# Optimization experiments

Measured on AMD Instinct MI355X. Metric: run time of the kernel, lower is better.

## Reference

```python
import jax, jax.numpy as jnp
import numpy as np

EPS = 1e-5

def layer_norm(x, g, b):
    mu = jnp.mean(x, axis=-1, keepdims=True)
    var = jnp.mean((x - mu) ** 2, axis=-1, keepdims=True)
    return (x - mu) * jax.lax.rsqrt(var + EPS) * g + b

def lstm_scan(x, Wih, Whh, bih, bhh, H):
    # x: [B, T, D]; PyTorch gate order i, f, g, o
    B = x.shape[0]
    gx = jnp.einsum('btd,gd->btg', x, Wih) + bih  # [B, T, 4H]
    gx = jnp.transpose(gx, (1, 0, 2))             # [T, B, 4H]
    def step(carry, g_t):
        h, c = carry
        g = g_t + h @ Whh.T + bhh
        i, f, gg, o = jnp.split(g, 4, axis=-1)
        c = jax.nn.sigmoid(f) * c + jax.nn.sigmoid(i) * jnp.tanh(gg)
        h = jax.nn.sigmoid(o) * jnp.tanh(c)
        return (h, c), h
    h0 = jnp.zeros((B, H), x.dtype)
    (_, _), hs = jax.lax.scan(step, (h0, h0), gx)
    return jnp.transpose(hs, (1, 0, 2))  # [B, T, H]

def gru_last(x, Wih, Whh, bih, bhh, H):
    # x: [B, T, D]; PyTorch gate order r, z, n; returns final hidden [B, H]
    B = x.shape[0]
    gx = jnp.einsum('btd,gd->btg', x, Wih) + bih  # [B, T, 3H]
    gx = jnp.transpose(gx, (1, 0, 2))             # [T, B, 3H]
    def step(h, g_t):
        gh = h @ Whh.T + bhh
        gxr, gxz, gxn = jnp.split(g_t, 3, axis=-1)
        ghr, ghz, ghn = jnp.split(gh, 3, axis=-1)
        r = jax.nn.sigmoid(gxr + ghr)
        z = jax.nn.sigmoid(gxz + ghz)
        n = jnp.tanh(gxn + r * ghn)
        h = (1.0 - z) * n + z * h
        return h, None
    h0 = jnp.zeros((B, H), x.dtype)
    h_last, _ = jax.lax.scan(step, h0, gx)
    return h_last

def setup_inputs() -> dict:
    key = jax.random.key(0)
    ks = jax.random.split(key, 16)
    B, T, D = 512, 512, 128
    H, G, F, C = 128, 128, 160, 64
    s = lambda n: 1.0 / np.sqrt(n)
    u = lambda k, shape, n: jax.random.uniform(k, shape, jnp.float32, -s(n), s(n))
    return {
        'x': jax.random.normal(ks[0], (B, T, D), jnp.float32),
        'lstm_Wih': u(ks[1], (4 * H, D), H), 'lstm_Whh': u(ks[2], (4 * H, H), H),
        'lstm_bih': u(ks[3], (4 * H,), H), 'lstm_bhh': u(ks[4], (4 * H,), H),
        'gru_Wih': u(ks[5], (3 * G, H), G), 'gru_Whh': u(ks[6], (3 * G, G), G),
        'gru_bih': u(ks[7], (3 * G,), G), 'gru_bhh': u(ks[8], (3 * G,), G),
        'ln_lstm_g': jnp.ones((H,), jnp.float32), 'ln_lstm_b': jnp.zeros((H,), jnp.float32),
        'ln_gru_g': jnp.ones((G,), jnp.float32), 'ln_gru_b': jnp.zeros((G,), jnp.float32),
        'fc1_W': u(ks[9], (F, G), G), 'fc1_b': u(ks[10], (F,), G),
        'ln_fc1_g': jnp.ones((F,), jnp.float32), 'ln_fc1_b': jnp.zeros((F,), jnp.float32),
        'fco_W': u(ks[11], (C, F), F), 'fco_b': u(ks[12], (C,), F),
    }

def reference(x, lstm_Wih, lstm_Whh, lstm_bih, lstm_bhh,
              gru_Wih, gru_Whh, gru_bih, gru_bhh,
              ln_lstm_g, ln_lstm_b, ln_gru_g, ln_gru_b,
              fc1_W, fc1_b, ln_fc1_g, ln_fc1_b, fco_W, fco_b):
    H = lstm_Whh.shape[1]
    G = gru_Whh.shape[1]
    lstm_out = lstm_scan(x, lstm_Wih, lstm_Whh, lstm_bih, lstm_bhh, H)  # [B,T,H]
    lstm_out = layer_norm(lstm_out, ln_lstm_g, ln_lstm_b)  # dropout = identity (eval)
    h_last = gru_last(lstm_out, gru_Wih, gru_Whh, gru_bih, gru_bhh, G)  # [B,G]
    h_last = layer_norm(h_last, ln_gru_g, ln_gru_b)
    h_last = jax.nn.relu(h_last)
    z = h_last @ fc1_W.T + fc1_b
    z = jax.nn.relu(layer_norm(z, ln_fc1_g, ln_fc1_b))
    return z @ fco_W.T + fco_b
```

## Files before the change

kernel.cpp:

```cpp
#include <hip/hip_runtime.h>


typedef __attribute__((ext_vector_type(8))) short bf16x8;
typedef __attribute__((ext_vector_type(4))) float f32x4;
typedef __attribute__((ext_vector_type(4))) int i32x4;
typedef unsigned short u16;
typedef unsigned int u32;

#define TT 512
#define HSTR 136

__device__ __forceinline__ u16 f2bf(float f) {
  u32 u = __builtin_bit_cast(u32, f);
  u += 0x7fffu + ((u >> 16) & 1u);
  return (u16)(u >> 16);
}
__device__ __forceinline__ float bf2f(u16 h) {
  return __builtin_bit_cast(float, (u32)h << 16);
}
__device__ __forceinline__ u32 packbf2(float a, float b) {
  return (u32)f2bf(a) | ((u32)f2bf(b) << 16);
}
__device__ __forceinline__ bf16x8 ldg8(const u16* p) {
  return __builtin_bit_cast(bf16x8, *(const i32x4*)p);
}
__device__ __forceinline__ float frcp(float x) { return __builtin_amdgcn_rcpf(x); }
__device__ __forceinline__ float sigm(float x) { return frcp(1.f + __expf(-x)); }
__device__ __forceinline__ float tanh_f(float x) {
  return 1.f - 2.f * frcp(__expf(2.f * x) + 1.f);
}
__device__ __forceinline__ void scan_barrier() {
  __asm__ volatile("" ::: "memory");
  __builtin_amdgcn_s_waitcnt(0xC07F);
  __builtin_amdgcn_s_barrier();
  __asm__ volatile("" ::: "memory");
}
__device__ __forceinline__ void acc_stats(bf16x8 v, float& s1, float& s2) {
#pragma unroll
  for (int j = 0; j < 8; j++) {
    float f = bf2f((u16)v[j]);
    s1 += f;
    s2 = __builtin_fmaf(f, f, s2);
  }
}

__global__ void prep_x(const float* __restrict__ x, u16* __restrict__ xb) {
  size_t i = ((size_t)blockIdx.x * 256 + threadIdx.x) * 4;
  float4 v = *(const float4*)(x + i);
  *(uint2*)(xb + i) = make_uint2(packbf2(v.x, v.y), packbf2(v.z, v.w));
}

__global__ void prep_misc(
    const float* __restrict__ wihl, const float* __restrict__ whhl,
    const float* __restrict__ wihg, const float* __restrict__ whhg,
    const float* __restrict__ bihl, const float* __restrict__ bhhl,
    const float* __restrict__ fc1W, const float* __restrict__ fcoW,
    const float* __restrict__ lnLg, const float* __restrict__ lnLb,
    u16* __restrict__ wihlb, u16* __restrict__ whhlb,
    u16* __restrict__ wihgb, u16* __restrict__ whhgb,
    float* __restrict__ biasl, float* __restrict__ fc1Wt, float* __restrict__ fcoWt,
    float* __restrict__ s1v, float* __restrict__ s2v, u32* __restrict__ flags) {
  int i = blockIdx.x * 256 + threadIdx.x;
  if (i < 65536) {
    wihlb[i] = f2bf(wihl[i]);
  } else if (i < 131072) {
    int k = i - 65536; whhlb[k] = f2bf(whhl[k]);
  } else if (i < 180224) {
    int k = i - 131072;
    wihgb[k] = f2bf(wihg[k] * lnLg[k & 127]);
  } else if (i < 229376) {
    int k = i - 180224; whhgb[k] = f2bf(whhg[k]);
  } else if (i < 229888) {
    int k = i - 229376; biasl[k] = bihl[k] + bhhl[k];
  } else if (i < 250368) {
    int k = i - 229888;
    fc1Wt[k] = fc1W[(k % 160) * 128 + (k / 160)];
  } else if (i < 260608) {
    int k = i - 250368;
    fcoWt[k] = fcoW[(k % 64) * 160 + (k / 64)];
  } else if (i < 260992) {
    int r = i - 260608;
    const float* wr = wihg + r * 128;
    float a = 0.f, b = 0.f;
    for (int j = 0; j < 128; j++) { a += wr[j] * lnLg[j]; b += wr[j] * lnLb[j]; }
    s1v[r] = a; s2v[r] = b;
  } else if (i < 261120) {
    flags[i - 260992] = 0;
  }
}

__global__ __launch_bounds__(512, 2) void scan_pair(
    const u16* __restrict__ xbf,
    const u16* __restrict__ whhl,
    const u16* __restrict__ wihl,
    const float* __restrict__ biasl,
    u16* __restrict__ lout,
    const u16* __restrict__ whhg,
    const u16* __restrict__ wihg,
    const float* __restrict__ gbih, const float* __restrict__ gbhh,
    const float* __restrict__ s1v, const float* __restrict__ s2v,
    float* __restrict__ hlast,
    u32* __restrict__ flags) {
  const int tid = threadIdx.x;
  const int w = tid >> 6, l = tid & 63;
  const int hc = l & 15, q = l >> 4;
  const int col = w * 16 + hc;
  const int pid = blockIdx.x;
  const int grp = ((pid >> 4) << 3) | (pid & 7);
  const int role = (pid >> 3) & 1;
  const int b0 = grp * 4;
  const int mrow = q * 4;
  const int hbase = hc * HSTR + q * 8;

  __shared__ __align__(16) u16 hb0[16 * HSTR];
  __shared__ __align__(16) u16 hb1[16 * HSTR];
  __shared__ float2 stats[2][16];

  for (int i = tid; i < 16 * HSTR; i += 512) { hb0[i] = 0; hb1[i] = 0; }

  if (role == 0) {
    bf16x8 wfh[4][4], wfx[4][4];
#pragma unroll
    for (int g = 0; g < 4; g++)
#pragma unroll
      for (int k0 = 0; k0 < 4; k0++) {
        wfh[g][k0] = ldg8(&whhl[(g * 128 + col) * 128 + k0 * 32 + q * 8]);
        wfx[g][k0] = ldg8(&wihl[(g * 128 + col) * 128 + k0 * 32 + q * 8]);
      }
    float bsl[4];
#pragma unroll
    for (int g = 0; g < 4; g++) bsl[g] = biasl[g * 128 + col];

    float c = 0.f;
    u32 loff = (u32)(b0 + q) * (TT * 128) + col;
    const u32 xbase = (u32)(b0 + (hc >> 2)) * (TT * 128) + (u32)(hc & 3) * 128 + q * 8;

    f32x4 axA[4], axB[4];
    bf16x8 xf[4];
    {
      bf16x8 f0[4];
#pragma unroll
      for (int k0 = 0; k0 < 4; k0++) f0[k0] = ldg8(&xbf[xbase + k0 * 32]);
#pragma unroll
      for (int g = 0; g < 4; g++) axA[g] = (f32x4){0.f, 0.f, 0.f, 0.f};
#pragma unroll
      for (int k0 = 0; k0 < 4; k0++)
#pragma unroll
        for (int g = 0; g < 4; g++)
          axA[g] = __builtin_amdgcn_mfma_f32_16x16x32_bf16(f0[k0], wfx[g][k0], axA[g], 0, 0, 0);
    }
#pragma unroll
    for (int k0 = 0; k0 < 4; k0++) xf[k0] = ldg8(&xbf[xbase + 512 + k0 * 32]);
    u32 xload = xbase + 1024;
    scan_barrier();

    auto step = [&](int s, f32x4 (&axc)[4], f32x4 (&axn)[4],
                    const u16* hrd, u16* hwr) {
      bf16x8 af[4];
#pragma unroll
      for (int k0 = 0; k0 < 4; k0++) af[k0] = ldg8(&hrd[hbase + k0 * 32]);
      f32x4 ah[4];
#pragma unroll
      for (int g = 0; g < 4; g++) ah[g] = (f32x4){0.f, 0.f, 0.f, 0.f};
#pragma unroll
      for (int k0 = 0; k0 < 4; k0++)
#pragma unroll
        for (int g = 0; g < 4; g++)
          ah[g] = __builtin_amdgcn_mfma_f32_16x16x32_bf16(af[k0], wfh[g][k0], ah[g], 0, 0, 0);
      float pi = ah[0][0] + axc[0][s] + bsl[0];
      float pf = ah[1][0] + axc[1][s] + bsl[1];
      float pg = ah[2][0] + axc[2][s] + bsl[2];
      float po = ah[3][0] + axc[3][s] + bsl[3];
      c = sigm(pf) * c + sigm(pi) * tanh_f(pg);
      float h = sigm(po) * tanh_f(c);
      u16 hv = f2bf(h);
      hwr[mrow * HSTR + col] = hv;
      lout[loff] = hv;
      loff += 128;
#pragma unroll
      for (int g = 0; g < 4; g++)
        axn[g] = __builtin_amdgcn_mfma_f32_16x16x32_bf16(xf[s], wfx[g][s], axn[g], 0, 0, 0);
      scan_barrier();
    };

    auto group = [&](f32x4 (&axc)[4], f32x4 (&axn)[4], u32 rel) {
#pragma unroll
      for (int g = 0; g < 4; g++) axn[g] = (f32x4){0.f, 0.f, 0.f, 0.f};
      step(0, axc, axn, hb0, hb1);
      step(1, axc, axn, hb1, hb0);
      step(2, axc, axn, hb0, hb1);
      step(3, axc, axn, hb1, hb0);
      if (rel) {
        __builtin_amdgcn_s_waitcnt(0x0070);
        __builtin_amdgcn_s_barrier();
        if (tid == 0)
          __hip_atomic_store(flags + grp, rel, __ATOMIC_RELEASE, __HIP_MEMORY_SCOPE_AGENT);
      }
#pragma unroll
      for (int k0 = 0; k0 < 4; k0++) xf[k0] = ldg8(&xbf[xload + k0 * 32]);
      xload += 512;
    };

#pragma unroll 1
    for (int tg = 0; tg < TT; tg += 8) {
      group(axA, axB, 0u);
      group(axB, axA, (tg & 8) ? (u32)(tg + 8) : 0u);
    }
    __builtin_amdgcn_s_waitcnt(0x0070);
    __builtin_amdgcn_s_barrier();
    if (tid == 0)
      __hip_atomic_store(flags + grp, (u32)TT, __ATOMIC_RELEASE, __HIP_MEMORY_SCOPE_AGENT);

  } else {
    bf16x8 wfh[3][4], wfx[3][4];
#pragma unroll
    for (int g = 0; g < 3; g++)
#pragma unroll
      for (int k0 = 0; k0 < 4; k0++) {
        wfh[g][k0] = ldg8(&whhg[(g * 128 + col) * 128 + k0 * 32 + q * 8]);
        wfx[g][k0] = ldg8(&wihg[(g * 128 + col) * 128 + k0 * 32 + q * 8]);
      }
    float s1g[3];
#pragma unroll
    for (int g = 0; g < 3; g++) s1g[g] = s1v[g * 128 + col];
    const float brz = gbih[col] + gbhh[col] + s2v[col];
    const float bzz = gbih[128 + col] + gbhh[128 + col] + s2v[128 + col];
    const float bnx = gbih[256 + col] + s2v[256 + col];
    const float bnh = gbhh[256 + col];

    float hp = 0.f;
    const u32 xbase = (u32)(b0 + (hc >> 2)) * (TT * 128) + (u32)(hc & 3) * 128 + q * 8;
    float s1a = 0.f, s2a = 0.f;
    u32 seen = 0;

    while (seen < 8) {
      seen = __hip_atomic_load(flags + grp, __ATOMIC_ACQUIRE, __HIP_MEMORY_SCOPE_AGENT);
      if (seen < 8) __builtin_amdgcn_s_sleep(8);
    }

    f32x4 axA[3], axB[3];
    bf16x8 xf[4];
    {
      bf16x8 f0[4];
#pragma unroll
      for (int k0 = 0; k0 < 4; k0++) f0[k0] = ldg8(&lout[xbase + k0 * 32]);
#pragma unroll
      for (int g = 0; g < 3; g++) axA[g] = (f32x4){0.f, 0.f, 0.f, 0.f};
#pragma unroll
      for (int k0 = 0; k0 < 4; k0++)
#pragma unroll
        for (int g = 0; g < 3; g++)
          axA[g] = __builtin_amdgcn_mfma_f32_16x16x32_bf16(f0[k0], wfx[g][k0], axA[g], 0, 0, 0);
      float a1 = 0.f, a2 = 0.f;
#pragma unroll
      for (int k0 = 0; k0 < 4; k0++) acc_stats(f0[k0], a1, a2);
      a1 += __shfl_xor(a1, 16); a1 += __shfl_xor(a1, 32);
      a2 += __shfl_xor(a2, 16); a2 += __shfl_xor(a2, 32);
      float mu = a1 * 0.0078125f;
      float var = a2 * 0.0078125f - mu * mu;
      float rsv = rsqrtf(var + 1e-5f);
      if (w == 0 && q == 0) stats[0][hc] = make_float2(mu, rsv);
    }
#pragma unroll
    for (int k0 = 0; k0 < 4; k0++) xf[k0] = ldg8(&lout[xbase + 512 + k0 * 32]);
    u32 xload = xbase + 1024;
    scan_barrier();

    auto step = [&](int s, f32x4 (&axc)[3], f32x4 (&axn)[3],
                    const u16* hrd, u16* hwr, int rdslot) {
      bf16x8 af[4];
#pragma unroll
      for (int k0 = 0; k0 < 4; k0++) af[k0] = ldg8(&hrd[hbase + k0 * 32]);
      f32x4 ah[3];
#pragma unroll
      for (int g = 0; g < 3; g++) ah[g] = (f32x4){0.f, 0.f, 0.f, 0.f};
#pragma unroll
      for (int k0 = 0; k0 < 4; k0++)
#pragma unroll
        for (int g = 0; g < 3; g++)
          ah[g] = __builtin_amdgcn_mfma_f32_16x16x32_bf16(af[k0], wfh[g][k0], ah[g], 0, 0, 0);
      const float2 st = stats[rdslot][4 * q + s];
      const float rsu = st.x * st.y;
      float ax0 = st.y * axc[0][s] - rsu * s1g[0];
      float ax1 = st.y * axc[1][s] - rsu * s1g[1];
      float ax2 = st.y * axc[2][s] - rsu * s1g[2];
      float rr = sigm(ax0 + ah[0][0] + brz);
      float zz = sigm(ax1 + ah[1][0] + bzz);
      float nn = tanh_f(ax2 + bnx + rr * (ah[2][0] + bnh));
      hp = nn + zz * (hp - nn);
      hwr[mrow * HSTR + col] = f2bf(hp);
#pragma unroll
      for (int g = 0; g < 3; g++)
        axn[g] = __builtin_amdgcn_mfma_f32_16x16x32_bf16(xf[s], wfx[g][s], axn[g], 0, 0, 0);
      acc_stats(xf[s], s1a, s2a);
      if (s == 3) {
        float t1 = s1a + __shfl_xor(s1a, 16); t1 += __shfl_xor(t1, 32);
        float t2 = s2a + __shfl_xor(s2a, 16); t2 += __shfl_xor(t2, 32);
        float mu = t1 * 0.0078125f;
        float var = t2 * 0.0078125f - mu * mu;
        float rsv = rsqrtf(var + 1e-5f);
        if (w == 0 && q == 0) stats[rdslot ^ 1][hc] = make_float2(mu, rsv);
        s1a = 0.f; s2a = 0.f;
      }
      scan_barrier();
    };

    auto group = [&](f32x4 (&axc)[3], f32x4 (&axn)[3], int rdslot) {
#pragma unroll
      for (int g = 0; g < 3; g++) axn[g] = (f32x4){0.f, 0.f, 0.f, 0.f};
      step(0, axc, axn, hb0, hb1, rdslot);
      step(1, axc, axn, hb1, hb0, rdslot);
      step(2, axc, axn, hb0, hb1, rdslot);
      step(3, axc, axn, hb1, hb0, rdslot);
#pragma unroll
      for (int k0 = 0; k0 < 4; k0++) xf[k0] = ldg8(&lout[xload + k0 * 32]);
      xload += 512;
    };

#pragma unroll 1
    for (int tg = 0; tg < TT; tg += 8) {
      u32 need = (u32)(tg + 16) > (u32)TT ? (u32)TT : (u32)(tg + 16);
      if (seen < need) {
        do {
          seen = __hip_atomic_load(flags + grp, __ATOMIC_ACQUIRE, __HIP_MEMORY_SCOPE_AGENT);
          if (seen < need) __builtin_amdgcn_s_sleep(8);
        } while (seen < need);
      }
      group(axA, axB, (tg >> 2) & 1);
      group(axB, axA, ((tg >> 2) + 1) & 1);
    }
    hlast[(size_t)(b0 + q) * 128 + col] = hp;
  }
}

__global__ __launch_bounds__(256) void head(
    const float* __restrict__ hlast,
    const float* __restrict__ g1, const float* __restrict__ b1,
    const float* __restrict__ fc1Wt, const float* __restrict__ fc1b,
    const float* __restrict__ g2, const float* __restrict__ b2,
    const float* __restrict__ fcoWt, const float* __restrict__ fcob,
    float* __restrict__ out) {
  const int b = blockIdx.x, tid = threadIdx.x;
  __shared__ float yv[128];
  __shared__ float zv[160];
  __shared__ float red[8];
  float v = (tid < 128) ? hlast[b * 128 + tid] : 0.f;
  float p1 = v, p2 = v * v;
#pragma unroll
  for (int m = 1; m < 64; m <<= 1) { p1 += __shfl_xor(p1, m); p2 += __shfl_xor(p2, m); }
  if ((tid & 63) == 0) { red[(tid >> 6) * 2] = p1; red[(tid >> 6) * 2 + 1] = p2; }
  __syncthreads();
  float s1 = red[0] + red[2] + red[4] + red[6];
  float s2 = red[1] + red[3] + red[5] + red[7];
  float mean = s1 * (1.f / 128.f);
  float var = s2 * (1.f / 128.f) - mean * mean;
  float rs = rsqrtf(var + 1e-5f);
  if (tid < 128) yv[tid] = fmaxf((v - mean) * rs * g1[tid] + b1[tid], 0.f);
  __syncthreads();
  float z = 0.f;
  if (tid < 160) {
    z = fc1b[tid];
    for (int g = 0; g < 128; g++) z += yv[g] * fc1Wt[g * 160 + tid];
  }
  float q1 = (tid < 160) ? z : 0.f;
  float q2 = (tid < 160) ? z * z : 0.f;
#pragma unroll
  for (int m = 1; m < 64; m <<= 1) { q1 += __shfl_xor(q1, m); q2 += __shfl_xor(q2, m); }
  __syncthreads();
  if ((tid & 63) == 0) { red[(tid >> 6) * 2] = q1; red[(tid >> 6) * 2 + 1] = q2; }
  __syncthreads();
  s1 = red[0] + red[2] + red[4] + red[6];
  s2 = red[1] + red[3] + red[5] + red[7];
  mean = s1 * (1.f / 160.f);
  var = s2 * (1.f / 160.f) - mean * mean;
  rs = rsqrtf(var + 1e-5f);
  if (tid < 160) zv[tid] = fmaxf((z - mean) * rs * g2[tid] + b2[tid], 0.f);
  __syncthreads();
  if (tid < 64) {
    float o = fcob[tid];
    for (int f = 0; f < 160; f++) o += zv[f] * fcoWt[f * 64 + tid];
    out[b * 64 + tid] = o;
  }
}

static constexpr size_t OFF_XBF   = 0;
static constexpr size_t OFF_LOUT  = 67108864;
static constexpr size_t OFF_WIHL  = OFF_LOUT + 67108864;
static constexpr size_t OFF_WHHL  = OFF_WIHL + 131072;
static constexpr size_t OFF_WIHG  = OFF_WHHL + 131072;
static constexpr size_t OFF_WHHG  = OFF_WIHG + 98304;
static constexpr size_t OFF_BIASL = OFF_WHHG + 98304;
static constexpr size_t OFF_FC1T  = OFF_BIASL + 2048;
static constexpr size_t OFF_FCOT  = OFF_FC1T + 81920;
static constexpr size_t OFF_HLAST = OFF_FCOT + 40960;
static constexpr size_t OFF_S1    = OFF_HLAST + 262144;
static constexpr size_t OFF_S2    = OFF_S1 + 1536;
static constexpr size_t OFF_FLAGS = OFF_S2 + 1536;

extern "C" void kernel_launch(void* const* d_in, const int* in_sizes, int n_in,
                              void* d_out, int out_size, void* d_ws, size_t ws_size,
                              hipStream_t stream) {
  (void)in_sizes; (void)n_in; (void)out_size; (void)ws_size;
  const float* x    = (const float*)d_in[0];
  const float* lWih = (const float*)d_in[1];
  const float* lWhh = (const float*)d_in[2];
  const float* lbih = (const float*)d_in[3];
  const float* lbhh = (const float*)d_in[4];
  const float* gWih = (const float*)d_in[5];
  const float* gWhh = (const float*)d_in[6];
  const float* gbih = (const float*)d_in[7];
  const float* gbhh = (const float*)d_in[8];
  const float* lnLg = (const float*)d_in[9];
  const float* lnLb = (const float*)d_in[10];
  const float* lnGg = (const float*)d_in[11];
  const float* lnGb = (const float*)d_in[12];
  const float* fc1W = (const float*)d_in[13];
  const float* fc1b = (const float*)d_in[14];
  const float* lnFg = (const float*)d_in[15];
  const float* lnFb = (const float*)d_in[16];
  const float* fcoW = (const float*)d_in[17];
  const float* fcob = (const float*)d_in[18];

  char* ws = (char*)d_ws;
  u16* xbf     = (u16*)(ws + OFF_XBF);
  u16* lout    = (u16*)(ws + OFF_LOUT);
  u16* wihlb   = (u16*)(ws + OFF_WIHL);
  u16* whhlb   = (u16*)(ws + OFF_WHHL);
  u16* wihgb   = (u16*)(ws + OFF_WIHG);
  u16* whhgb   = (u16*)(ws + OFF_WHHG);
  float* biasl = (float*)(ws + OFF_BIASL);
  float* fc1Wt = (float*)(ws + OFF_FC1T);
  float* fcoWt = (float*)(ws + OFF_FCOT);
  float* hlast = (float*)(ws + OFF_HLAST);
  float* s1v   = (float*)(ws + OFF_S1);
  float* s2v   = (float*)(ws + OFF_S2);
  u32* flags   = (u32*)(ws + OFF_FLAGS);
  float* out   = (float*)d_out;

  prep_x<<<32768, 256, 0, stream>>>(x, xbf);
  prep_misc<<<1024, 256, 0, stream>>>(lWih, lWhh, gWih, gWhh, lbih, lbhh, fc1W, fcoW,
                                      lnLg, lnLb,
                                      wihlb, whhlb, wihgb, whhgb, biasl, fc1Wt, fcoWt,
                                      s1v, s2v, flags);
  scan_pair<<<256, 512, 0, stream>>>(xbf, whhlb, wihlb, biasl, lout,
                                     whhgb, wihgb, gbih, gbhh, s1v, s2v,
                                     hlast, flags);
  head<<<512, 256, 0, stream>>>(hlast, lnGg, lnGb, fc1Wt, fc1b, lnFg, lnFb, fcoWt, fcob, out);
}
```

Measured before the change: 648.0 us.

## Fuse x bf16 conversion and head MLP into the scan kernel

Drops the separate prep_x launch: the LSTM role now loads fp32 x directly and packs it to bf16 in registers. It also drops the separate head kernel, so the GRU role runs layernorm, fc1, layernorm and the output projection in shared memory right after its scan. A guard stops the x prefetch from reading past the end of the sequence. This saves a full 128MB read+write pass and two launches, at the cost of twice the global bytes per x load inside the latency-critical scan loop.

```diff
diff --git a/kernel.cpp b/kernel.cpp
--- a/kernel.cpp
+++ b/kernel.cpp
@@ -24,6 +24,16 @@
 __device__ __forceinline__ bf16x8 ldg8(const u16* p) {
   return __builtin_bit_cast(bf16x8, *(const i32x4*)p);
 }
+__device__ __forceinline__ bf16x8 ldx8(const float* p) {
+  const float4 v0 = *(const float4*)p;
+  const float4 v1 = *(const float4*)(p + 4);
+  i32x4 r;
+  r[0] = (int)packbf2(v0.x, v0.y);
+  r[1] = (int)packbf2(v0.z, v0.w);
+  r[2] = (int)packbf2(v1.x, v1.y);
+  r[3] = (int)packbf2(v1.z, v1.w);
+  return __builtin_bit_cast(bf16x8, r);
+}
 __device__ __forceinline__ float frcp(float x) { return __builtin_amdgcn_rcpf(x); }
 __device__ __forceinline__ float sigm(float x) { return frcp(1.f + __expf(-x)); }
 __device__ __forceinline__ float tanh_f(float x) {
@@ -42,12 +52,6 @@
     s1 += f;
     s2 = __builtin_fmaf(f, f, s2);
   }
-}
-
-__global__ void prep_x(const float* __restrict__ x, u16* __restrict__ xb) {
-  size_t i = ((size_t)blockIdx.x * 256 + threadIdx.x) * 4;
-  float4 v = *(const float4*)(x + i);
-  *(uint2*)(xb + i) = make_uint2(packbf2(v.x, v.y), packbf2(v.z, v.w));
 }
 
 __global__ void prep_misc(
@@ -90,7 +94,7 @@
 }
 
 __global__ __launch_bounds__(512, 2) void scan_pair(
-    const u16* __restrict__ xbf,
+    const float* __restrict__ x,
     const u16* __restrict__ whhl,
     const u16* __restrict__ wihl,
     const float* __restrict__ biasl,
@@ -99,8 +103,12 @@
     const u16* __restrict__ wihg,
     const float* __restrict__ gbih, const float* __restrict__ gbhh,
     const float* __restrict__ s1v, const float* __restrict__ s2v,
-    float* __restrict__ hlast,
-    u32* __restrict__ flags) {
+    u32* __restrict__ flags,
+    const float* __restrict__ lnGg, const float* __restrict__ lnGb,
+    const float* __restrict__ fc1Wt, const float* __restrict__ fc1b,
+    const float* __restrict__ lnFg, const float* __restrict__ lnFb,
+    const float* __restrict__ fcoWt, const float* __restrict__ fcob,
+    float* __restrict__ out) {
   const int tid = threadIdx.x;
   const int w = tid >> 6, l = tid & 63;
   const int hc = l & 15, q = l >> 4;
@@ -115,6 +123,8 @@
   __shared__ __align__(16) u16 hb0[16 * HSTR];
   __shared__ __align__(16) u16 hb1[16 * HSTR];
   __shared__ float2 stats[2][16];
+  __shared__ float hl[4][128];
+  __shared__ float zl[4][160];
 
   for (int i = tid; i < 16 * HSTR; i += 512) { hb0[i] = 0; hb1[i] = 0; }
 
@@ -140,7 +150,7 @@
     {
       bf16x8 f0[4];
 #pragma unroll
-      for (int k0 = 0; k0 < 4; k0++) f0[k0] = ldg8(&xbf[xbase + k0 * 32]);
+      for (int k0 = 0; k0 < 4; k0++) f0[k0] = ldx8(&x[xbase + k0 * 32]);
 #pragma unroll
       for (int g = 0; g < 4; g++) axA[g] = (f32x4){0.f, 0.f, 0.f, 0.f};
 #pragma unroll
@@ -150,7 +160,7 @@
           axA[g] = __builtin_amdgcn_mfma_f32_16x16x32_bf16(f0[k0], wfx[g][k0], axA[g], 0, 0, 0);
     }
 #pragma unroll
-    for (int k0 = 0; k0 < 4; k0++) xf[k0] = ldg8(&xbf[xbase + 512 + k0 * 32]);
+    for (int k0 = 0; k0 < 4; k0++) xf[k0] = ldx8(&x[xbase + 512 + k0 * 32]);
     u32 xload = xbase + 1024;
     scan_barrier();
 
@@ -183,7 +193,7 @@
       scan_barrier();
     };
 
-    auto group = [&](f32x4 (&axc)[4], f32x4 (&axn)[4], u32 rel) {
+    auto group = [&](f32x4 (&axc)[4], f32x4 (&axn)[4], u32 rel, int kk) {
 #pragma unroll
       for (int g = 0; g < 4; g++) axn[g] = (f32x4){0.f, 0.f, 0.f, 0.f};
       step(0, axc, axn, hb0, hb1);
@@ -196,15 +206,18 @@
         if (tid == 0)
           __hip_atomic_store(flags + grp, rel, __ATOMIC_RELEASE, __HIP_MEMORY_SCOPE_AGENT);
       }
-#pragma unroll
-      for (int k0 = 0; k0 < 4; k0++) xf[k0] = ldg8(&xbf[xload + k0 * 32]);
-      xload += 512;
+      if (kk <= 125) {
+#pragma unroll
+        for (int k0 = 0; k0 < 4; k0++) xf[k0] = ldx8(&x[xload + k0 * 32]);
+        xload += 512;
+      }
     };
 
 #pragma unroll 1
     for (int tg = 0; tg < TT; tg += 8) {
-      group(axA, axB, 0u);
-      group(axB, axA, (tg & 8) ? (u32)(tg + 8) : 0u);
+      const int kk = tg >> 2;
+      group(axA, axB, 0u, kk);
+      group(axB, axA, (tg & 8) ? (u32)(tg + 8) : 0u, kk + 1);
     }
     __builtin_amdgcn_s_waitcnt(0x0070);
     __builtin_amdgcn_s_barrier();
@@ -329,62 +342,55 @@
       group(axA, axB, (tg >> 2) & 1);
       group(axB, axA, ((tg >> 2) + 1) & 1);
     }
-    hlast[(size_t)(b0 + q) * 128 + col] = hp;
+
+    hl[q][col] = hp;
+    __syncthreads();
+    if (tid < 256) {
+      const int u = tid >> 6, ln = tid & 63;
+      float a0 = hl[u][ln], a1 = hl[u][ln + 64];
+      float s1 = a0 + a1, s2 = a0 * a0 + a1 * a1;
+#pragma unroll
+      for (int m = 1; m < 64; m <<= 1) { s1 += __shfl_xor(s1, m); s2 += __shfl_xor(s2, m); }
+      float mean = s1 * 0.0078125f;
+      float var = s2 * 0.0078125f - mean * mean;
+      float rs = rsqrtf(var + 1e-5f);
+      hl[u][ln]      = fmaxf((a0 - mean) * rs * lnGg[ln] + lnGb[ln], 0.f);
+      hl[u][ln + 64] = fmaxf((a1 - mean) * rs * lnGg[ln + 64] + lnGb[ln + 64], 0.f);
+    }
+    __syncthreads();
+    for (int idx = tid; idx < 640; idx += 512) {
+      const int u = idx / 160, f = idx - u * 160;
+      float z = fc1b[f];
+      for (int g = 0; g < 128; g++) z = __builtin_fmaf(hl[u][g], fc1Wt[g * 160 + f], z);
+      zl[u][f] = z;
+    }
+    __syncthreads();
+    if (tid < 256) {
+      const int u = tid >> 6, ln = tid & 63;
+      float v0 = zl[u][ln], v1 = zl[u][ln + 64];
+      float v2 = (ln < 32) ? zl[u][ln + 128] : 0.f;
+      float s1 = v0 + v1 + v2, s2 = v0 * v0 + v1 * v1 + v2 * v2;
+#pragma unroll
+      for (int m = 1; m < 64; m <<= 1) { s1 += __shfl_xor(s1, m); s2 += __shfl_xor(s2, m); }
+      float mean = s1 * (1.f / 160.f);
+      float var = s2 * (1.f / 160.f) - mean * mean;
+      float rs = rsqrtf(var + 1e-5f);
+      zl[u][ln]      = fmaxf((v0 - mean) * rs * lnFg[ln] + lnFb[ln], 0.f);
+      zl[u][ln + 64] = fmaxf((v1 - mean) * rs * lnFg[ln + 64] + lnFb[ln + 64], 0.f);
+      if (ln < 32)
+        zl[u][ln + 128] = fmaxf((v2 - mean) * rs * lnFg[ln + 128] + lnFb[ln + 128], 0.f);
+    }
+    __syncthreads();
+    if (tid < 256) {
+      const int u = tid >> 6, cc = tid & 63;
+      float o = fcob[cc];
+      for (int f = 0; f < 160; f++) o = __builtin_fmaf(zl[u][f], fcoWt[f * 64 + cc], o);
+      out[(size_t)(b0 + u) * 64 + cc] = o;
+    }
   }
 }
 
-__global__ __launch_bounds__(256) void head(
-    const float* __restrict__ hlast,
-    const float* __restrict__ g1, const float* __restrict__ b1,
-    const float* __restrict__ fc1Wt, const float* __restrict__ fc1b,
-    const float* __restrict__ g2, const float* __restrict__ b2,
-    const float* __restrict__ fcoWt, const float* __restrict__ fcob,
-    float* __restrict__ out) {
-  const int b = blockIdx.x, tid = threadIdx.x;
-  __shared__ float yv[128];
-  __shared__ float zv[160];
-  __shared__ float red[8];
-  float v = (tid < 128) ? hlast[b * 128 + tid] : 0.f;
-  float p1 = v, p2 = v * v;
-#pragma unroll
-  for (int m = 1; m < 64; m <<= 1) { p1 += __shfl_xor(p1, m); p2 += __shfl_xor(p2, m); }
-  if ((tid & 63) == 0) { red[(tid >> 6) * 2] = p1; red[(tid >> 6) * 2 + 1] = p2; }
-  __syncthreads();
-  float s1 = red[0] + red[2] + red[4] + red[6];
-  float s2 = red[1] + red[3] + red[5] + red[7];
-  float mean = s1 * (1.f / 128.f);
-  float var = s2 * (1.f / 128.f) - mean * mean;
-  float rs = rsqrtf(var + 1e-5f);
-  if (tid < 128) yv[tid] = fmaxf((v - mean) * rs * g1[tid] + b1[tid], 0.f);
-  __syncthreads();
-  float z = 0.f;
-  if (tid < 160) {
-    z = fc1b[tid];
-    for (int g = 0; g < 128; g++) z += yv[g] * fc1Wt[g * 160 + tid];
-  }
-  float q1 = (tid < 160) ? z : 0.f;
-  float q2 = (tid < 160) ? z * z : 0.f;
-#pragma unroll
-  for (int m = 1; m < 64; m <<= 1) { q1 += __shfl_xor(q1, m); q2 += __shfl_xor(q2, m); }
-  __syncthreads();
-  if ((tid & 63) == 0) { red[(tid >> 6) * 2] = q1; red[(tid >> 6) * 2 + 1] = q2; }
-  __syncthreads();
-  s1 = red[0] + red[2] + red[4] + red[6];
-  s2 = red[1] + red[3] + red[5] + red[7];
-  mean = s1 * (1.f / 160.f);
-  var = s2 * (1.f / 160.f) - mean * mean;
-  rs = rsqrtf(var + 1e-5f);
-  if (tid < 160) zv[tid] = fmaxf((z - mean) * rs * g2[tid] + b2[tid], 0.f);
-  __syncthreads();
-  if (tid < 64) {
-    float o = fcob[tid];
-    for (int f = 0; f < 160; f++) o += zv[f] * fcoWt[f * 64 + tid];
-    out[b * 64 + tid] = o;
-  }
-}
-
-static constexpr size_t OFF_XBF   = 0;
-static constexpr size_t OFF_LOUT  = 67108864;
+static constexpr size_t OFF_LOUT  = 0;
 static constexpr size_t OFF_WIHL  = OFF_LOUT + 67108864;
 static constexpr size_t OFF_WHHL  = OFF_WIHL + 131072;
 static constexpr size_t OFF_WIHG  = OFF_WHHL + 131072;
@@ -392,8 +398,7 @@
 static constexpr size_t OFF_BIASL = OFF_WHHG + 98304;
 static constexpr size_t OFF_FC1T  = OFF_BIASL + 2048;
 static constexpr size_t OFF_FCOT  = OFF_FC1T + 81920;
-static constexpr size_t OFF_HLAST = OFF_FCOT + 40960;
-static constexpr size_t OFF_S1    = OFF_HLAST + 262144;
+static constexpr size_t OFF_S1    = OFF_FCOT + 40960;
 static constexpr size_t OFF_S2    = OFF_S1 + 1536;
 static constexpr size_t OFF_FLAGS = OFF_S2 + 1536;
 
@@ -422,7 +427,6 @@
   const float* fcob = (const float*)d_in[18];
 
   char* ws = (char*)d_ws;
-  u16* xbf     = (u16*)(ws + OFF_XBF);
   u16* lout    = (u16*)(ws + OFF_LOUT);
   u16* wihlb   = (u16*)(ws + OFF_WIHL);
   u16* whhlb   = (u16*)(ws + OFF_WHHL);
@@ -431,19 +435,17 @@
   float* biasl = (float*)(ws + OFF_BIASL);
   float* fc1Wt = (float*)(ws + OFF_FC1T);
   float* fcoWt = (float*)(ws + OFF_FCOT);
-  float* hlast = (float*)(ws + OFF_HLAST);
   float* s1v   = (float*)(ws + OFF_S1);
   float* s2v   = (float*)(ws + OFF_S2);
   u32* flags   = (u32*)(ws + OFF_FLAGS);
   float* out   = (float*)d_out;
 
-  prep_x<<<32768, 256, 0, stream>>>(x, xbf);
   prep_misc<<<1024, 256, 0, stream>>>(lWih, lWhh, gWih, gWhh, lbih, lbhh, fc1W, fcoW,
                                       lnLg, lnLb,
                                       wihlb, whhlb, wihgb, whhgb, biasl, fc1Wt, fcoWt,
                                       s1v, s2v, flags);
-  scan_pair<<<256, 512, 0, stream>>>(xbf, whhlb, wihlb, biasl, lout,
-                                     whhgb, wihgb, gbih, gbhh, s1v, s2v,
-                                     hlast, flags);
-  head<<<512, 256, 0, stream>>>(hlast, lnGg, lnGb, fc1Wt, fc1b, lnFg, lnFb, fcoWt, fcob, out);
-}
+  scan_pair<<<256, 512, 0, stream>>>(x, whhlb, wihlb, biasl, lout,
+                                     whhgb, wihgb, gbih, gbhh, s1v, s2v, flags,
+                                     lnGg, lnGb, fc1Wt, fc1b, lnFg, lnFb, fcoWt, fcob,
+                                     out);
+}
```

Measured after the change: 827.4 us. 1.28x slower.
